# Optimization experiments

Hardware: AMD Instinct MI355X
Metric: run time of the kernel (lower is better)

The kernel has to match this reference:

```python
import jax, jax.numpy as jnp
import numpy as np

B, N, XD = 4, 8192, 256   # batch, seq len, input/kv feature dim
F, H = 512, 8             # features, heads
D = F // H                # per-head dim = 64
EPS = 1e-6                # flax LayerNorm default epsilon


def _layer_norm(t, scale, bias):
    mu = jnp.mean(t, axis=-1, keepdims=True)
    var = jnp.mean(jnp.square(t - mu), axis=-1, keepdims=True)
    return (t - mu) * jax.lax.rsqrt(var + EPS) * scale + bias


def setup_inputs() -> dict:
    key = jax.random.key(0)
    ks = jax.random.split(key, 5)
    return {
        "x": jax.random.normal(ks[0], (B, N, XD), jnp.float32),
        "kv": jax.random.normal(ks[1], (B, N, XD), jnp.float32),
        # linen.initializers.normal(1/x_dim) / normal(1/h_dim)
        "Q": jax.random.normal(ks[2], (XD, F), jnp.float32) * (1.0 / XD),
        "K": jax.random.normal(ks[3], (XD, F), jnp.float32) * (1.0 / XD),
        "V": jax.random.normal(ks[4], (XD, F), jnp.float32) * (1.0 / XD),
        "log_scale": jnp.zeros((F,), jnp.float32),
        "ln_q_scale": jnp.ones((D,), jnp.float32),
        "ln_q_bias": jnp.zeros((D,), jnp.float32),
        "ln_k_scale": jnp.ones((D,), jnp.float32),
        "ln_k_bias": jnp.zeros((D,), jnp.float32),
        "ln_v_scale": jnp.ones((D,), jnp.float32),
        "ln_v_bias": jnp.zeros((D,), jnp.float32),
    }


def reference(x, kv, Q, K, V, log_scale,
              ln_q_scale, ln_q_bias, ln_k_scale, ln_k_bias, ln_v_scale, ln_v_bias):
    # QKV projections (value scaled by exp(log_scale) per feature)
    query = x @ Q                                    # [B, N, F]
    key = kv @ K                                     # [B, N, F]
    value = jnp.exp(log_scale) * (kv @ V)            # [B, N, F]
    # reshape exactly as the source module does
    q = query.reshape(B, H, -1, D)                   # [B, H, N, D]
    k = key.reshape(B, H, -1, D)
    v = value.reshape(B, H, -1, D)
    # per-head LayerNorm over the head dim (layer_norm=True)
    q = _layer_norm(q, ln_q_scale, ln_q_bias)
    k = _layer_norm(k, ln_k_scale, ln_k_bias)
    v = _layer_norm(v, ln_v_scale, ln_v_bias)
    # galerkin linear attention: Q @ (K^T V) / seq_len, no softmax, no NxN scores
    seq_len = k.shape[-2]
    ctx = jnp.einsum('bhnd,bhne->bhde', k, v)        # [B, H, D, D]
    out = jnp.einsum('bhnd,bhde->bhne', q, ctx) / seq_len
    return out.reshape(B, N, F)
```

## Files before the change

kernel.cpp:

```cpp
#include <hip/hip_runtime.h>
#include <stdint.h>

using f32x4  = __attribute__((ext_vector_type(4))) float;
using short8 = __attribute__((ext_vector_type(8))) short;
using u16x4  = __attribute__((ext_vector_type(4))) unsigned short;

#define MFMA(a, b, c) __builtin_amdgcn_mfma_f32_16x16x32_bf16((a), (b), (c), 0, 0, 0)

#define XDIM 256
#define FDIM 512
#define EPS  1e-6f

#define QT_OFF    0u
#define KT_OFF    262144u
#define VT_OFF    524288u
#define CTXT_OFF  786432u
#define PART_OFF  1048576u

static __device__ __forceinline__ unsigned short f2bf(float f) {
  unsigned u = __float_as_uint(f);
  unsigned r = u + 0x7FFFu + ((u >> 16) & 1u);
  return (unsigned short)(r >> 16);
}

static __device__ __forceinline__ void stage_a_full(const float* a_rows, int tid, char* Alds) {
  const int r = tid >> 2, cq = tid & 3;
  const float* src = a_rows + (size_t)r * XDIM + cq * 64;
  char* dst = Alds + r * 528 + cq * 128;
#pragma unroll
  for (int i = 0; i < 4; ++i) {
    float4 f0 = *(const float4*)(src + i * 16);
    float4 f1 = *(const float4*)(src + i * 16 + 4);
    float4 f2 = *(const float4*)(src + i * 16 + 8);
    float4 f3 = *(const float4*)(src + i * 16 + 12);
    short8 v0, v1;
    v0[0] = (short)f2bf(f0.x); v0[1] = (short)f2bf(f0.y);
    v0[2] = (short)f2bf(f0.z); v0[3] = (short)f2bf(f0.w);
    v0[4] = (short)f2bf(f1.x); v0[5] = (short)f2bf(f1.y);
    v0[6] = (short)f2bf(f1.z); v0[7] = (short)f2bf(f1.w);
    v1[0] = (short)f2bf(f2.x); v1[1] = (short)f2bf(f2.y);
    v1[2] = (short)f2bf(f2.z); v1[3] = (short)f2bf(f2.w);
    v1[4] = (short)f2bf(f3.x); v1[5] = (short)f2bf(f3.y);
    v1[6] = (short)f2bf(f3.z); v1[7] = (short)f2bf(f3.w);
    *(short8*)(dst + i * 32)      = v0;
    *(short8*)(dst + i * 32 + 16) = v1;
  }
}

static __device__ __forceinline__ void load_bphase(const char* base, int ks, int lr, int koff,
                                                   short8 b[8]) {
#pragma unroll
  for (int nt = 0; nt < 4; ++nt) {
    const char* r = base + (size_t)(nt * 16 + lr) * 512 + ks * 128 + koff;
    b[nt * 2]     = *(const short8*)(r);
    b[nt * 2 + 1] = *(const short8*)(r + 64);
  }
}

static __device__ __forceinline__ void chunk_layernorm(f32x4 acc[4][4], const float* sc,
                                                       const float* bs, int lane) {
  const int lr = lane & 15;
  float scl[4], bia[4];
#pragma unroll
  for (int nt = 0; nt < 4; ++nt) { scl[nt] = sc[nt * 16 + lr]; bia[nt] = bs[nt * 16 + lr]; }
#pragma unroll
  for (int mt = 0; mt < 4; ++mt) {
#pragma unroll
    for (int j = 0; j < 4; ++j) {
      float a0 = acc[mt][0][j], a1 = acc[mt][1][j], a2 = acc[mt][2][j], a3 = acc[mt][3][j];
      float s  = a0 + a1 + a2 + a3;
      float s2 = a0 * a0 + a1 * a1 + a2 * a2 + a3 * a3;
#pragma unroll
      for (int off = 1; off < 16; off <<= 1) {
        s  += __shfl_xor(s, off, 16);
        s2 += __shfl_xor(s2, off, 16);
      }
      const float mu  = s * (1.0f / 64.0f);
      const float var = s2 * (1.0f / 64.0f) - mu * mu;
      const float rs  = rsqrtf(var + EPS);
#pragma unroll
      for (int nt = 0; nt < 4; ++nt)
        acc[mt][nt][j] = (acc[mt][nt][j] - mu) * rs * scl[nt] + bia[nt];
    }
  }
}

__global__ void prep_weights_kernel(const float* __restrict__ Q, const float* __restrict__ K,
                                    const float* __restrict__ V, const float* __restrict__ ls,
                                    unsigned short* __restrict__ Qt, unsigned short* __restrict__ Kt,
                                    unsigned short* __restrict__ Vt) {
  const int flat = blockIdx.x * 256 + threadIdx.x;
  const int mat = flat >> 17;
  const int rem = flat & 131071;
  const int f = rem & 511;
  const int k = rem >> 9;
  if (mat == 0)      Qt[f * 256 + k] = f2bf(Q[k * 512 + f]);
  else if (mat == 1) Kt[f * 256 + k] = f2bf(K[k * 512 + f]);
  else               Vt[f * 256 + k] = f2bf(V[k * 512 + f] * expf(ls[f]));
}

__launch_bounds__(256, 2)
__global__ void kv_ctx_kernel(const float* __restrict__ kv,
                              const unsigned short* __restrict__ Kt,
                              const unsigned short* __restrict__ Vt,
                              const float* __restrict__ lnk_s, const float* __restrict__ lnk_b,
                              const float* __restrict__ lnv_s, const float* __restrict__ lnv_b,
                              float* __restrict__ partials) {
  __shared__ __align__(16) char smem[33792];

  const int tid = threadIdx.x, lane = tid & 63, w = tid >> 6;
  const int bid = blockIdx.x, rb = bid >> 1, nb = bid & 1;
  const int row0 = rb * 64;
  const int lr = lane & 15, lk = lane >> 4;
  const int koff = lk * 16;

  stage_a_full(kv + (size_t)row0 * XDIM, tid, smem);

  const f32x4 z4 = {0.f, 0.f, 0.f, 0.f};
  f32x4 acck[4][4], accv[4][4];
#pragma unroll
  for (int i = 0; i < 4; ++i)
#pragma unroll
    for (int j = 0; j < 4; ++j) { acck[i][j] = z4; accv[i][j] = z4; }

  const char* kbase = (const char*)Kt + (size_t)(nb * 256 + w * 64) * 512;
  const char* vbase = (const char*)Vt + (size_t)(nb * 256 + w * 64) * 512;

  short8 bufK[8], bufV[8];
  load_bphase(kbase, 0, lr, koff, bufK);
  load_bphase(vbase, 0, lr, koff, bufV);

  __syncthreads();

#pragma unroll
  for (int ks = 0; ks < 4; ++ks) {
    short8 a0[4], a1[4];
#pragma unroll
    for (int mt = 0; mt < 4; ++mt) {
      const char* ar = smem + (mt * 16 + lr) * 528 + ks * 128;
      a0[mt] = *(const short8*)(ar + koff);
      a1[mt] = *(const short8*)(ar + 64 + koff);
    }
#pragma unroll
    for (int mt = 0; mt < 4; ++mt)
#pragma unroll
      for (int nt = 0; nt < 4; ++nt) {
        acck[mt][nt] = MFMA(a0[mt], bufK[nt * 2],     acck[mt][nt]);
        acck[mt][nt] = MFMA(a1[mt], bufK[nt * 2 + 1], acck[mt][nt]);
      }
    if (ks < 3) load_bphase(kbase, ks + 1, lr, koff, bufK);
#pragma unroll
    for (int mt = 0; mt < 4; ++mt)
#pragma unroll
      for (int nt = 0; nt < 4; ++nt) {
        accv[mt][nt] = MFMA(a0[mt], bufV[nt * 2],     accv[mt][nt]);
        accv[mt][nt] = MFMA(a1[mt], bufV[nt * 2 + 1], accv[mt][nt]);
      }
    if (ks < 3) load_bphase(vbase, ks + 1, lr, koff, bufV);
  }

  chunk_layernorm(acck, lnk_s, lnk_b, lane);
  chunk_layernorm(accv, lnv_s, lnv_b, lane);

  char* knT = smem;
  char* vnT = smem + 16384;
  f32x4 cacc[4];
#pragma unroll
  for (int i = 0; i < 4; ++i) cacc[i] = z4;
  const int drow = w * 16 + lr;

#pragma unroll
  for (int half = 0; half < 2; ++half) {
    __syncthreads();
    if ((w >> 1) == half) {
      const int tb2 = (w & 1) * 128;
#pragma unroll
      for (int mt = 0; mt < 4; ++mt) {
        const int tb = tb2 + mt * 32 + lk * 8;
#pragma unroll
        for (int nt = 0; nt < 4; ++nt) {
          const int d = nt * 16 + lr;
          u16x4 pk, pv;
#pragma unroll
          for (int j = 0; j < 4; ++j) {
            pk[j] = f2bf(acck[mt][nt][j]);
            pv[j] = f2bf(accv[mt][nt][j]);
          }
          const int boff = d * 256 + (tb ^ ((d & 7) << 4));
          *(u16x4*)(knT + boff) = pk;
          *(u16x4*)(vnT + boff) = pv;
        }
      }
    }
    __syncthreads();
#pragma unroll
    for (int s = 0; s < 4; ++s) {
      const short8 a = *(const short8*)(knT + drow * 256 + ((s * 64 + koff) ^ ((drow & 7) << 4)));
#pragma unroll
      for (int nt = 0; nt < 4; ++nt) {
        const int e = nt * 16 + lr;
        const short8 b = *(const short8*)(vnT + e * 256 + ((s * 64 + koff) ^ ((e & 7) << 4)));
        cacc[nt] = MFMA(a, b, cacc[nt]);
      }
    }
  }

  float* pout = partials + (size_t)bid * 4096;
#pragma unroll
  for (int nt = 0; nt < 4; ++nt)
#pragma unroll
    for (int j = 0; j < 4; ++j)
      pout[(w * 16 + lk * 4 + j) * 64 + nt * 16 + lr] = cacc[nt][j];
}

__global__ void reduce_ctx_kernel(const float* __restrict__ partials,
                                  unsigned short* __restrict__ ctxTg) {
  const int bid = blockIdx.x, t = threadIdx.x;
  const int gg = bid >> 3, sl = bid & 7;
  const float* base = partials + (size_t)gg * 32 * 4096;
#pragma unroll
  for (int rep = 0; rep < 2; ++rep) {
    const int idx = sl * 512 + rep * 256 + t;
    float acc = 0.f;
#pragma unroll 8
    for (int p = 0; p < 32; ++p) acc += base[(size_t)p * 4096 + idx];
    const int d = idx >> 6, e = idx & 63;
    ctxTg[(size_t)gg * 4096 + e * 64 + d] = f2bf(acc * (1.0f / 8192.0f));
  }
}

__launch_bounds__(256, 3)
__global__ void q_out_kernel(const float* __restrict__ x, const unsigned short* __restrict__ Qt,
                             const unsigned short* __restrict__ ctxTg,
                             const float* __restrict__ lnq_s, const float* __restrict__ lnq_b,
                             float* __restrict__ out) {
  __shared__ __align__(16) char smem[43008];

  const int tid = threadIdx.x, lane = tid & 63, w = tid >> 6;
  const int bid = blockIdx.x, rb = bid >> 1, nb = bid & 1;
  const int row0 = rb * 64;
  const int g = row0 >> 10;
  const int lr = lane & 15, lk = lane >> 4;
  const int koff = lk * 16;
  char* ctxT = smem + 33792;

  stage_a_full(x + (size_t)row0 * XDIM, tid, smem);

  {
    const unsigned short* src = ctxTg + (size_t)g * 4096 + (tid >> 2) * 64 + (tid & 3) * 16;
    char* dst = ctxT + (tid >> 2) * 144 + (tid & 3) * 32;
    *(short8*)dst        = *(const short8*)(src);
    *(short8*)(dst + 16) = *(const short8*)(src + 8);
  }

  const f32x4 z4 = {0.f, 0.f, 0.f, 0.f};
  f32x4 acc[4][4];
#pragma unroll
  for (int i = 0; i < 4; ++i)
#pragma unroll
    for (int j = 0; j < 4; ++j) acc[i][j] = z4;

  const char* qbase = (const char*)Qt + (size_t)(nb * 256 + w * 64) * 512;

  __syncthreads();

#pragma unroll
  for (int ks = 0; ks < 4; ++ks) {
    short8 b0[8];
    load_bphase(qbase, ks, lr, koff, b0);
    short8 a0[4], a1[4];
#pragma unroll
    for (int mt = 0; mt < 4; ++mt) {
      const char* ar = smem + (mt * 16 + lr) * 528 + ks * 128;
      a0[mt] = *(const short8*)(ar + koff);
      a1[mt] = *(const short8*)(ar + 64 + koff);
    }
#pragma unroll
    for (int mt = 0; mt < 4; ++mt)
#pragma unroll
      for (int nt = 0; nt < 4; ++nt)
        acc[mt][nt] = MFMA(a0[mt], b0[nt * 2], acc[mt][nt]);
#pragma unroll
    for (int mt = 0; mt < 4; ++mt)
#pragma unroll
      for (int nt = 0; nt < 4; ++nt)
        acc[mt][nt] = MFMA(a1[mt], b0[nt * 2 + 1], acc[mt][nt]);
  }

  chunk_layernorm(acc, lnq_s, lnq_b, lane);

  __syncthreads();

  char* A2 = smem + w * 8192;
#pragma unroll
  for (int mt = 0; mt < 4; ++mt)
#pragma unroll
    for (int j = 0; j < 4; ++j) {
      const int m = mt * 16 + lk * 4 + j;
      const int sw = (m & 7) << 4;
#pragma unroll
      for (int nt = 0; nt < 4; ++nt) {
        const int d = nt * 16 + lr;
        *(unsigned short*)(A2 + m * 128 + ((d * 2) ^ sw)) = f2bf(acc[mt][nt][j]);
      }
    }
  __syncthreads();

  f32x4 o[4][4];
#pragma unroll
  for (int i = 0; i < 4; ++i)
#pragma unroll
    for (int j = 0; j < 4; ++j) o[i][j] = z4;

#pragma unroll
  for (int s = 0; s < 2; ++s) {
    short8 a[4], b[4];
#pragma unroll
    for (int mt = 0; mt < 4; ++mt) {
      const int m = mt * 16 + lr;
      a[mt] = *(const short8*)(A2 + m * 128 + ((s * 64 + koff) ^ ((m & 7) << 4)));
    }
#pragma unroll
    for (int nt = 0; nt < 4; ++nt)
      b[nt] = *(const short8*)(ctxT + (nt * 16 + lr) * 144 + s * 64 + koff);
#pragma unroll
    for (int mt = 0; mt < 4; ++mt)
#pragma unroll
      for (int nt = 0; nt < 4; ++nt)
        o[mt][nt] = MFMA(a[mt], b[nt], o[mt][nt]);
  }

#pragma unroll
  for (int mt = 0; mt < 4; ++mt)
#pragma unroll
    for (int nt = 0; nt < 4; ++nt)
#pragma unroll
      for (int j = 0; j < 4; ++j) {
        const int n = mt * 16 + lk * 4 + j;
        out[(size_t)(row0 + n) * FDIM + nb * 256 + w * 64 + nt * 16 + lr] = o[mt][nt][j];
      }
}

extern "C" void kernel_launch(void* const* d_in, const int* in_sizes, int n_in,
                              void* d_out, int out_size, void* d_ws, size_t ws_size,
                              hipStream_t stream) {
  (void)in_sizes; (void)n_in; (void)out_size; (void)ws_size;
  const float* x     = (const float*)d_in[0];
  const float* kv    = (const float*)d_in[1];
  const float* Q     = (const float*)d_in[2];
  const float* K     = (const float*)d_in[3];
  const float* V     = (const float*)d_in[4];
  const float* ls    = (const float*)d_in[5];
  const float* lnq_s = (const float*)d_in[6];
  const float* lnq_b = (const float*)d_in[7];
  const float* lnk_s = (const float*)d_in[8];
  const float* lnk_b = (const float*)d_in[9];
  const float* lnv_s = (const float*)d_in[10];
  const float* lnv_b = (const float*)d_in[11];
  float* out = (float*)d_out;

  char* ws = (char*)d_ws;
  unsigned short* Qt   = (unsigned short*)(ws + QT_OFF);
  unsigned short* Kt   = (unsigned short*)(ws + KT_OFF);
  unsigned short* Vt   = (unsigned short*)(ws + VT_OFF);
  unsigned short* ctxT = (unsigned short*)(ws + CTXT_OFF);
  float* partials      = (float*)(ws + PART_OFF);

  prep_weights_kernel<<<1536, 256, 0, stream>>>(Q, K, V, ls, Qt, Kt, Vt);
  kv_ctx_kernel<<<1024, 256, 0, stream>>>(kv, Kt, Vt, lnk_s, lnk_b, lnv_s, lnv_b, partials);
  reduce_ctx_kernel<<<256, 256, 0, stream>>>(partials, ctxT);
  q_out_kernel<<<1024, 256, 0, stream>>>(x, Qt, ctxT, lnq_s, lnq_b, out);
}
```

Before: 111.6 us.

## Pre-convert activations to swizzled bf16 and stage them via async global-to-LDS loads

A prep pass now converts x and kv to bf16 in a swizzled row layout in the workspace. The projection kernels then stage rows straight into LDS with global_load_lds instead of converting fp32 per block. Tiles are split across 2x2 waves over 128-column slices, which doubles the grid and allows higher occupancy. In exchange it adds an extra full read and write of the activations in a separate pass, and doubles the partials that the reduction has to sum.

```diff
diff --git a/kernel.cpp b/kernel.cpp
--- a/kernel.cpp
+++ b/kernel.cpp
@@ -6,6 +6,8 @@
 using u16x4  = __attribute__((ext_vector_type(4))) unsigned short;
 
 #define MFMA(a, b, c) __builtin_amdgcn_mfma_f32_16x16x32_bf16((a), (b), (c), 0, 0, 0)
+#define GLOBAL_AS __attribute__((address_space(1)))
+#define LDS_AS    __attribute__((address_space(3)))
 
 #define XDIM 256
 #define FDIM 512
@@ -15,7 +17,9 @@
 #define KT_OFF    262144u
 #define VT_OFF    524288u
 #define CTXT_OFF  786432u
-#define PART_OFF  1048576u
+#define KVB_OFF   1048576u
+#define XB_OFF    17825792u
+#define PART_OFF  34603008u
 
 static __device__ __forceinline__ unsigned short f2bf(float f) {
   unsigned u = __float_as_uint(f);
@@ -23,48 +27,29 @@
   return (unsigned short)(r >> 16);
 }
 
-static __device__ __forceinline__ void stage_a_full(const float* a_rows, int tid, char* Alds) {
-  const int r = tid >> 2, cq = tid & 3;
-  const float* src = a_rows + (size_t)r * XDIM + cq * 64;
-  char* dst = Alds + r * 528 + cq * 128;
-#pragma unroll
-  for (int i = 0; i < 4; ++i) {
-    float4 f0 = *(const float4*)(src + i * 16);
-    float4 f1 = *(const float4*)(src + i * 16 + 4);
-    float4 f2 = *(const float4*)(src + i * 16 + 8);
-    float4 f3 = *(const float4*)(src + i * 16 + 12);
-    short8 v0, v1;
-    v0[0] = (short)f2bf(f0.x); v0[1] = (short)f2bf(f0.y);
-    v0[2] = (short)f2bf(f0.z); v0[3] = (short)f2bf(f0.w);
-    v0[4] = (short)f2bf(f1.x); v0[5] = (short)f2bf(f1.y);
-    v0[6] = (short)f2bf(f1.z); v0[7] = (short)f2bf(f1.w);
-    v1[0] = (short)f2bf(f2.x); v1[1] = (short)f2bf(f2.y);
-    v1[2] = (short)f2bf(f2.z); v1[3] = (short)f2bf(f2.w);
-    v1[4] = (short)f2bf(f3.x); v1[5] = (short)f2bf(f3.y);
-    v1[6] = (short)f2bf(f3.z); v1[7] = (short)f2bf(f3.w);
-    *(short8*)(dst + i * 32)      = v0;
-    *(short8*)(dst + i * 32 + 16) = v1;
-  }
-}
-
-static __device__ __forceinline__ void load_bphase(const char* base, int ks, int lr, int koff,
-                                                   short8 b[8]) {
-#pragma unroll
-  for (int nt = 0; nt < 4; ++nt) {
-    const char* r = base + (size_t)(nt * 16 + lr) * 512 + ks * 128 + koff;
-    b[nt * 2]     = *(const short8*)(r);
-    b[nt * 2 + 1] = *(const short8*)(r + 64);
-  }
-}
-
-static __device__ __forceinline__ void chunk_layernorm(f32x4 acc[4][4], const float* sc,
+static __device__ __forceinline__ void async_copy16(const void* g, void* l) {
+  __builtin_amdgcn_global_load_lds((GLOBAL_AS const void*)g, (LDS_AS void*)l, 16, 0, 0);
+}
+
+static __device__ __forceinline__ void stage_a_async(const unsigned short* src_rows,
+                                                     int w, int lane, char* Alds) {
+#pragma unroll
+  for (int i = 0; i < 8; ++i) {
+    const int r = w * 16 + i * 2 + (lane >> 5);
+    async_copy16(src_rows + (size_t)r * 256 + (lane & 31) * 8,
+                 Alds + (w * 8 + i) * 1024);
+  }
+}
+
+template <int M_REP>
+static __device__ __forceinline__ void chunk_layernorm(f32x4 acc[M_REP][4], const float* sc,
                                                        const float* bs, int lane) {
   const int lr = lane & 15;
   float scl[4], bia[4];
 #pragma unroll
   for (int nt = 0; nt < 4; ++nt) { scl[nt] = sc[nt * 16 + lr]; bia[nt] = bs[nt * 16 + lr]; }
 #pragma unroll
-  for (int mt = 0; mt < 4; ++mt) {
+  for (int mt = 0; mt < M_REP; ++mt) {
 #pragma unroll
     for (int j = 0; j < 4; ++j) {
       float a0 = acc[mt][0][j], a1 = acc[mt][1][j], a2 = acc[mt][2][j], a3 = acc[mt][3][j];
@@ -85,123 +70,141 @@
   }
 }
 
-__global__ void prep_weights_kernel(const float* __restrict__ Q, const float* __restrict__ K,
-                                    const float* __restrict__ V, const float* __restrict__ ls,
-                                    unsigned short* __restrict__ Qt, unsigned short* __restrict__ Kt,
-                                    unsigned short* __restrict__ Vt) {
-  const int flat = blockIdx.x * 256 + threadIdx.x;
-  const int mat = flat >> 17;
-  const int rem = flat & 131071;
-  const int f = rem & 511;
-  const int k = rem >> 9;
-  if (mat == 0)      Qt[f * 256 + k] = f2bf(Q[k * 512 + f]);
-  else if (mat == 1) Kt[f * 256 + k] = f2bf(K[k * 512 + f]);
-  else               Vt[f * 256 + k] = f2bf(V[k * 512 + f] * expf(ls[f]));
-}
-
-__launch_bounds__(256, 2)
-__global__ void kv_ctx_kernel(const float* __restrict__ kv,
+__global__ void prep_kernel(const float* __restrict__ kv, const float* __restrict__ x,
+                            const float* __restrict__ Q, const float* __restrict__ K,
+                            const float* __restrict__ V, const float* __restrict__ ls,
+                            unsigned short* __restrict__ kvb, unsigned short* __restrict__ xb,
+                            unsigned short* __restrict__ Qt, unsigned short* __restrict__ Kt,
+                            unsigned short* __restrict__ Vt) {
+  const int bid = blockIdx.x, tid = threadIdx.x;
+  if (bid < 4096) {
+    const int sel = bid >> 11;
+    const float* src = sel ? x : kv;
+    unsigned short* dst = sel ? xb : kvb;
+    const size_t e16 = ((size_t)(bid & 2047) * 256 + tid) * 16;
+    const int row = (int)(e16 >> 8);
+    const int col = (int)(e16 & 255);
+    const int c0 = col >> 3;
+    const int s = row & 7;
+    const float* sp = src + e16;
+    short8 v0, v1;
+#pragma unroll
+    for (int j = 0; j < 8; ++j) v0[j] = (short)f2bf(sp[j]);
+#pragma unroll
+    for (int j = 0; j < 8; ++j) v1[j] = (short)f2bf(sp[8 + j]);
+    unsigned short* drow = dst + (size_t)row * 256;
+    *(short8*)(drow + ((c0 ^ s) << 3))       = v0;
+    *(short8*)(drow + (((c0 + 1) ^ s) << 3)) = v1;
+  } else {
+    const int flat = (bid - 4096) * 256 + tid;
+    const int mat = flat >> 17;
+    const int rem = flat & 131071;
+    const int f = rem & 511;
+    const int k = rem >> 9;
+    if (mat == 0)      Qt[f * 256 + k] = f2bf(Q[k * 512 + f]);
+    else if (mat == 1) Kt[f * 256 + k] = f2bf(K[k * 512 + f]);
+    else               Vt[f * 256 + k] = f2bf(V[k * 512 + f] * expf(ls[f]));
+  }
+}
+
+__launch_bounds__(256, 3)
+__global__ void kv_ctx_kernel(const unsigned short* __restrict__ kvb,
                               const unsigned short* __restrict__ Kt,
                               const unsigned short* __restrict__ Vt,
                               const float* __restrict__ lnk_s, const float* __restrict__ lnk_b,
                               const float* __restrict__ lnv_s, const float* __restrict__ lnv_b,
                               float* __restrict__ partials) {
-  __shared__ __align__(16) char smem[33792];
+  __shared__ __align__(16) char smem[32768];
 
   const int tid = threadIdx.x, lane = tid & 63, w = tid >> 6;
-  const int bid = blockIdx.x, rb = bid >> 1, nb = bid & 1;
+  const int wr = w >> 1, wc = w & 1;
+  const int bid = blockIdx.x, rb = bid >> 2, nb = bid & 3;
   const int row0 = rb * 64;
   const int lr = lane & 15, lk = lane >> 4;
-  const int koff = lk * 16;
-
-  stage_a_full(kv + (size_t)row0 * XDIM, tid, smem);
+
+  stage_a_async(kvb + (size_t)row0 * 256, w, lane, smem);
 
   const f32x4 z4 = {0.f, 0.f, 0.f, 0.f};
-  f32x4 acck[4][4], accv[4][4];
-#pragma unroll
-  for (int i = 0; i < 4; ++i)
+  f32x4 acck[2][4], accv[2][4];
+#pragma unroll
+  for (int i = 0; i < 2; ++i)
 #pragma unroll
     for (int j = 0; j < 4; ++j) { acck[i][j] = z4; accv[i][j] = z4; }
 
-  const char* kbase = (const char*)Kt + (size_t)(nb * 256 + w * 64) * 512;
-  const char* vbase = (const char*)Vt + (size_t)(nb * 256 + w * 64) * 512;
-
-  short8 bufK[8], bufV[8];
-  load_bphase(kbase, 0, lr, koff, bufK);
-  load_bphase(vbase, 0, lr, koff, bufV);
+  const unsigned short* kb = Kt + (size_t)(nb * 128 + wc * 64) * 256;
+  const unsigned short* vb = Vt + (size_t)(nb * 128 + wc * 64) * 256;
 
   __syncthreads();
 
 #pragma unroll
   for (int ks = 0; ks < 4; ++ks) {
-    short8 a0[4], a1[4];
-#pragma unroll
-    for (int mt = 0; mt < 4; ++mt) {
-      const char* ar = smem + (mt * 16 + lr) * 528 + ks * 128;
-      a0[mt] = *(const short8*)(ar + koff);
-      a1[mt] = *(const short8*)(ar + 64 + koff);
-    }
-#pragma unroll
-    for (int mt = 0; mt < 4; ++mt)
+    short8 bk[8], bv[8];
+#pragma unroll
+    for (int nt = 0; nt < 4; ++nt) {
+      const unsigned short* kr = kb + (size_t)(nt * 16 + lr) * 256 + ks * 64 + lk * 8;
+      const unsigned short* vr = vb + (size_t)(nt * 16 + lr) * 256 + ks * 64 + lk * 8;
+      bk[nt * 2] = *(const short8*)(kr); bk[nt * 2 + 1] = *(const short8*)(kr + 32);
+      bv[nt * 2] = *(const short8*)(vr); bv[nt * 2 + 1] = *(const short8*)(vr + 32);
+    }
+    short8 a0[2], a1[2];
+#pragma unroll
+    for (int mt = 0; mt < 2; ++mt) {
+      const int row = wr * 32 + mt * 16 + lr;
+      const int sw = (row & 7) << 4;
+      a0[mt] = *(const short8*)(smem + row * 512 + ((ks * 128 + lk * 16) ^ sw));
+      a1[mt] = *(const short8*)(smem + row * 512 + ((ks * 128 + 64 + lk * 16) ^ sw));
+    }
+#pragma unroll
+    for (int mt = 0; mt < 2; ++mt)
 #pragma unroll
       for (int nt = 0; nt < 4; ++nt) {
-        acck[mt][nt] = MFMA(a0[mt], bufK[nt * 2],     acck[mt][nt]);
-        acck[mt][nt] = MFMA(a1[mt], bufK[nt * 2 + 1], acck[mt][nt]);
-      }
-    if (ks < 3) load_bphase(kbase, ks + 1, lr, koff, bufK);
-#pragma unroll
-    for (int mt = 0; mt < 4; ++mt)
+        acck[mt][nt] = MFMA(a0[mt], bk[nt * 2],     acck[mt][nt]);
+        acck[mt][nt] = MFMA(a1[mt], bk[nt * 2 + 1], acck[mt][nt]);
+      }
+#pragma unroll
+    for (int mt = 0; mt < 2; ++mt)
 #pragma unroll
       for (int nt = 0; nt < 4; ++nt) {
-        accv[mt][nt] = MFMA(a0[mt], bufV[nt * 2],     accv[mt][nt]);
-        accv[mt][nt] = MFMA(a1[mt], bufV[nt * 2 + 1], accv[mt][nt]);
-      }
-    if (ks < 3) load_bphase(vbase, ks + 1, lr, koff, bufV);
-  }
-
-  chunk_layernorm(acck, lnk_s, lnk_b, lane);
-  chunk_layernorm(accv, lnv_s, lnv_b, lane);
+        accv[mt][nt] = MFMA(a0[mt], bv[nt * 2],     accv[mt][nt]);
+        accv[mt][nt] = MFMA(a1[mt], bv[nt * 2 + 1], accv[mt][nt]);
+      }
+  }
+
+  chunk_layernorm<2>(acck, lnk_s, lnk_b, lane);
+  chunk_layernorm<2>(accv, lnv_s, lnv_b, lane);
 
   char* knT = smem;
   char* vnT = smem + 16384;
+
+  __syncthreads();
+#pragma unroll
+  for (int mt = 0; mt < 2; ++mt) {
+    const int t = wc * 64 + wr * 32 + mt * 16 + lk * 4;
+#pragma unroll
+    for (int nt = 0; nt < 4; ++nt) {
+      const int d = nt * 16 + lr;
+      u16x4 pk, pv;
+#pragma unroll
+      for (int j = 0; j < 4; ++j) { pk[j] = f2bf(acck[mt][nt][j]); pv[j] = f2bf(accv[mt][nt][j]); }
+      const int boff = d * 256 + ((t * 2) ^ ((d & 7) << 4));
+      *(u16x4*)(knT + boff) = pk;
+      *(u16x4*)(vnT + boff) = pv;
+    }
+  }
+  __syncthreads();
+
   f32x4 cacc[4];
 #pragma unroll
   for (int i = 0; i < 4; ++i) cacc[i] = z4;
   const int drow = w * 16 + lr;
-
-#pragma unroll
-  for (int half = 0; half < 2; ++half) {
-    __syncthreads();
-    if ((w >> 1) == half) {
-      const int tb2 = (w & 1) * 128;
-#pragma unroll
-      for (int mt = 0; mt < 4; ++mt) {
-        const int tb = tb2 + mt * 32 + lk * 8;
-#pragma unroll
-        for (int nt = 0; nt < 4; ++nt) {
-          const int d = nt * 16 + lr;
-          u16x4 pk, pv;
-#pragma unroll
-          for (int j = 0; j < 4; ++j) {
-            pk[j] = f2bf(acck[mt][nt][j]);
-            pv[j] = f2bf(accv[mt][nt][j]);
-          }
-          const int boff = d * 256 + (tb ^ ((d & 7) << 4));
-          *(u16x4*)(knT + boff) = pk;
-          *(u16x4*)(vnT + boff) = pv;
-        }
-      }
-    }
-    __syncthreads();
-#pragma unroll
-    for (int s = 0; s < 4; ++s) {
-      const short8 a = *(const short8*)(knT + drow * 256 + ((s * 64 + koff) ^ ((drow & 7) << 4)));
-#pragma unroll
-      for (int nt = 0; nt < 4; ++nt) {
-        const int e = nt * 16 + lr;
-        const short8 b = *(const short8*)(vnT + e * 256 + ((s * 64 + koff) ^ ((e & 7) << 4)));
-        cacc[nt] = MFMA(a, b, cacc[nt]);
-      }
+#pragma unroll
+  for (int s = 0; s < 4; ++s) {
+    const short8 a = *(const short8*)(knT + drow * 256 + ((s * 64 + lk * 16) ^ ((drow & 7) << 4)));
+#pragma unroll
+    for (int nt = 0; nt < 4; ++nt) {
+      const int e = nt * 16 + lr;
+      const short8 b = *(const short8*)(vnT + e * 256 + ((s * 64 + lk * 16) ^ ((e & 7) << 4)));
+      cacc[nt] = MFMA(a, b, cacc[nt]);
     }
   }
 
@@ -217,127 +220,133 @@
                                   unsigned short* __restrict__ ctxTg) {
   const int bid = blockIdx.x, t = threadIdx.x;
   const int gg = bid >> 3, sl = bid & 7;
-  const float* base = partials + (size_t)gg * 32 * 4096;
+  const float* base = partials + (size_t)gg * 64 * 4096;
 #pragma unroll
   for (int rep = 0; rep < 2; ++rep) {
     const int idx = sl * 512 + rep * 256 + t;
     float acc = 0.f;
 #pragma unroll 8
-    for (int p = 0; p < 32; ++p) acc += base[(size_t)p * 4096 + idx];
+    for (int p = 0; p < 64; ++p) acc += base[(size_t)p * 4096 + idx];
     const int d = idx >> 6, e = idx & 63;
     ctxTg[(size_t)gg * 4096 + e * 64 + d] = f2bf(acc * (1.0f / 8192.0f));
   }
 }
 
-__launch_bounds__(256, 3)
-__global__ void q_out_kernel(const float* __restrict__ x, const unsigned short* __restrict__ Qt,
+__launch_bounds__(256, 4)
+__global__ void q_out_kernel(const unsigned short* __restrict__ xb,
+                             const unsigned short* __restrict__ Qt,
                              const unsigned short* __restrict__ ctxTg,
                              const float* __restrict__ lnq_s, const float* __restrict__ lnq_b,
                              float* __restrict__ out) {
-  __shared__ __align__(16) char smem[43008];
+  __shared__ __align__(16) char smem[32768];
 
   const int tid = threadIdx.x, lane = tid & 63, w = tid >> 6;
-  const int bid = blockIdx.x, rb = bid >> 1, nb = bid & 1;
+  const int wr = w >> 1, wc = w & 1;
+  const int bid = blockIdx.x, rb = bid >> 2, nb = bid & 3;
   const int row0 = rb * 64;
   const int g = row0 >> 10;
   const int lr = lane & 15, lk = lane >> 4;
-  const int koff = lk * 16;
-  char* ctxT = smem + 33792;
-
-  stage_a_full(x + (size_t)row0 * XDIM, tid, smem);
+
+  stage_a_async(xb + (size_t)row0 * 256, w, lane, smem);
+
+  const unsigned short* csrc = ctxTg + (size_t)g * 4096 + (tid >> 2) * 64 + (tid & 3) * 16;
+  const short8 c0 = *(const short8*)(csrc);
+  const short8 c1 = *(const short8*)(csrc + 8);
+
+  const f32x4 z4 = {0.f, 0.f, 0.f, 0.f};
+  f32x4 acc[2][4];
+#pragma unroll
+  for (int i = 0; i < 2; ++i)
+#pragma unroll
+    for (int j = 0; j < 4; ++j) acc[i][j] = z4;
+
+  const unsigned short* qb = Qt + (size_t)(nb * 128 + wc * 64) * 256;
+
+  __syncthreads();
+
+#pragma unroll
+  for (int ks = 0; ks < 4; ++ks) {
+    short8 bq[8];
+#pragma unroll
+    for (int nt = 0; nt < 4; ++nt) {
+      const unsigned short* qr = qb + (size_t)(nt * 16 + lr) * 256 + ks * 64 + lk * 8;
+      bq[nt * 2] = *(const short8*)(qr); bq[nt * 2 + 1] = *(const short8*)(qr + 32);
+    }
+    short8 a0[2], a1[2];
+#pragma unroll
+    for (int mt = 0; mt < 2; ++mt) {
+      const int row = wr * 32 + mt * 16 + lr;
+      const int sw = (row & 7) << 4;
+      a0[mt] = *(const short8*)(smem + row * 512 + ((ks * 128 + lk * 16) ^ sw));
+      a1[mt] = *(const short8*)(smem + row * 512 + ((ks * 128 + 64 + lk * 16) ^ sw));
+    }
+#pragma unroll
+    for (int mt = 0; mt < 2; ++mt)
+#pragma unroll
+      for (int nt = 0; nt < 4; ++nt) {
+        acc[mt][nt] = MFMA(a0[mt], bq[nt * 2],     acc[mt][nt]);
+        acc[mt][nt] = MFMA(a1[mt], bq[nt * 2 + 1], acc[mt][nt]);
+      }
+  }
+
+  chunk_layernorm<2>(acc, lnq_s, lnq_b, lane);
+
+  __syncthreads();
+
+  char* A2   = smem;
+  char* ctxT = smem + 16384;
 
   {
-    const unsigned short* src = ctxTg + (size_t)g * 4096 + (tid >> 2) * 64 + (tid & 3) * 16;
     char* dst = ctxT + (tid >> 2) * 144 + (tid & 3) * 32;
-    *(short8*)dst        = *(const short8*)(src);
-    *(short8*)(dst + 16) = *(const short8*)(src + 8);
-  }
-
-  const f32x4 z4 = {0.f, 0.f, 0.f, 0.f};
-  f32x4 acc[4][4];
-#pragma unroll
-  for (int i = 0; i < 4; ++i)
-#pragma unroll
-    for (int j = 0; j < 4; ++j) acc[i][j] = z4;
-
-  const char* qbase = (const char*)Qt + (size_t)(nb * 256 + w * 64) * 512;
-
-  __syncthreads();
-
-#pragma unroll
-  for (int ks = 0; ks < 4; ++ks) {
-    short8 b0[8];
-    load_bphase(qbase, ks, lr, koff, b0);
-    short8 a0[4], a1[4];
-#pragma unroll
-    for (int mt = 0; mt < 4; ++mt) {
-      const char* ar = smem + (mt * 16 + lr) * 528 + ks * 128;
-      a0[mt] = *(const short8*)(ar + koff);
-      a1[mt] = *(const short8*)(ar + 64 + koff);
-    }
-#pragma unroll
-    for (int mt = 0; mt < 4; ++mt)
-#pragma unroll
-      for (int nt = 0; nt < 4; ++nt)
-        acc[mt][nt] = MFMA(a0[mt], b0[nt * 2], acc[mt][nt]);
-#pragma unroll
-    for (int mt = 0; mt < 4; ++mt)
-#pragma unroll
-      for (int nt = 0; nt < 4; ++nt)
-        acc[mt][nt] = MFMA(a1[mt], b0[nt * 2 + 1], acc[mt][nt]);
-  }
-
-  chunk_layernorm(acc, lnq_s, lnq_b, lane);
-
-  __syncthreads();
-
-  char* A2 = smem + w * 8192;
-#pragma unroll
-  for (int mt = 0; mt < 4; ++mt)
+    *(short8*)dst        = c0;
+    *(short8*)(dst + 16) = c1;
+  }
+#pragma unroll
+  for (int mt = 0; mt < 2; ++mt)
 #pragma unroll
     for (int j = 0; j < 4; ++j) {
-      const int m = mt * 16 + lk * 4 + j;
+      const int m = wr * 32 + mt * 16 + lk * 4 + j;
       const int sw = (m & 7) << 4;
 #pragma unroll
       for (int nt = 0; nt < 4; ++nt) {
         const int d = nt * 16 + lr;
-        *(unsigned short*)(A2 + m * 128 + ((d * 2) ^ sw)) = f2bf(acc[mt][nt][j]);
-      }
-    }
-  __syncthreads();
-
-  f32x4 o[4][4];
-#pragma unroll
-  for (int i = 0; i < 4; ++i)
+        *(unsigned short*)(A2 + wc * 8192 + m * 128 + ((d * 2) ^ sw)) = f2bf(acc[mt][nt][j]);
+      }
+    }
+  __syncthreads();
+
+  f32x4 o[2][4];
+#pragma unroll
+  for (int i = 0; i < 2; ++i)
 #pragma unroll
     for (int j = 0; j < 4; ++j) o[i][j] = z4;
 
 #pragma unroll
   for (int s = 0; s < 2; ++s) {
-    short8 a[4], b[4];
-#pragma unroll
-    for (int mt = 0; mt < 4; ++mt) {
-      const int m = mt * 16 + lr;
-      a[mt] = *(const short8*)(A2 + m * 128 + ((s * 64 + koff) ^ ((m & 7) << 4)));
+    short8 a[2], b[4];
+#pragma unroll
+    for (int mt = 0; mt < 2; ++mt) {
+      const int m = wr * 32 + mt * 16 + lr;
+      a[mt] = *(const short8*)(A2 + wc * 8192 + m * 128 + ((s * 64 + lk * 16) ^ ((m & 7) << 4)));
     }
 #pragma unroll
     for (int nt = 0; nt < 4; ++nt)
-      b[nt] = *(const short8*)(ctxT + (nt * 16 + lr) * 144 + s * 64 + koff);
-#pragma unroll
-    for (int mt = 0; mt < 4; ++mt)
+      b[nt] = *(const short8*)(ctxT + (nt * 16 + lr) * 144 + s * 64 + lk * 16);
+#pragma unroll
+    for (int mt = 0; mt < 2; ++mt)
 #pragma unroll
       for (int nt = 0; nt < 4; ++nt)
         o[mt][nt] = MFMA(a[mt], b[nt], o[mt][nt]);
   }
 
 #pragma unroll
-  for (int mt = 0; mt < 4; ++mt)
+  for (int mt = 0; mt < 2; ++mt)
 #pragma unroll
     for (int nt = 0; nt < 4; ++nt)
 #pragma unroll
       for (int j = 0; j < 4; ++j) {
-        const int n = mt * 16 + lk * 4 + j;
-        out[(size_t)(row0 + n) * FDIM + nb * 256 + w * 64 + nt * 16 + lr] = o[mt][nt][j];
+        const int n = wr * 32 + mt * 16 + lk * 4 + j;
+        out[(size_t)(row0 + n) * FDIM + nb * 128 + wc * 64 + nt * 16 + lr] = o[mt][nt][j];
       }
 }
 
@@ -364,10 +373,12 @@
   unsigned short* Kt   = (unsigned short*)(ws + KT_OFF);
   unsigned short* Vt   = (unsigned short*)(ws + VT_OFF);
   unsigned short* ctxT = (unsigned short*)(ws + CTXT_OFF);
+  unsigned short* kvb  = (unsigned short*)(ws + KVB_OFF);
+  unsigned short* xb   = (unsigned short*)(ws + XB_OFF);
   float* partials      = (float*)(ws + PART_OFF);
 
-  prep_weights_kernel<<<1536, 256, 0, stream>>>(Q, K, V, ls, Qt, Kt, Vt);
-  kv_ctx_kernel<<<1024, 256, 0, stream>>>(kv, Kt, Vt, lnk_s, lnk_b, lnv_s, lnv_b, partials);
+  prep_kernel<<<5632, 256, 0, stream>>>(kv, x, Q, K, V, ls, kvb, xb, Qt, Kt, Vt);
+  kv_ctx_kernel<<<2048, 256, 0, stream>>>(kvb, Kt, Vt, lnk_s, lnk_b, lnv_s, lnv_b, partials);
   reduce_ctx_kernel<<<256, 256, 0, stream>>>(partials, ctxT);
-  q_out_kernel<<<1024, 256, 0, stream>>>(x, Qt, ctxT, lnq_s, lnq_b, out);
-}
+  q_out_kernel<<<2048, 256, 0, stream>>>(xb, Qt, ctxT, lnq_s, lnq_b, out);
+}
```

After: 149.7 us. +34.2%, slower.

## Make KV and Q kernels persistent over row tiles with register-prefetched staging

Applied to the files above, without the earlier changes.

Both main kernels now use 512-thread blocks that each loop over eight 64-row tiles instead of one. The next tile's fp32 input is prefetched into registers while MFMAs run on the current tile held in swizzled LDS. Each wave now covers 64 features, so a block spans 128 features. The weight B-fragments are cycled through registers each loop, and the partial context count per group halves, which shrinks the reduce kernel. The aims are to hide global-load latency, cut launch and block-setup overhead, and reduce partial-sum traffic. The cost is fewer blocks (256), so latency hiding relies on the in-loop prefetch and extra barriers per tile.

```diff
diff --git a/kernel.cpp b/kernel.cpp
--- a/kernel.cpp
+++ b/kernel.cpp
@@ -23,65 +23,51 @@
   return (unsigned short)(r >> 16);
 }
 
-static __device__ __forceinline__ void stage_a_full(const float* a_rows, int tid, char* Alds) {
-  const int r = tid >> 2, cq = tid & 3;
-  const float* src = a_rows + (size_t)r * XDIM + cq * 64;
-  char* dst = Alds + r * 528 + cq * 128;
-#pragma unroll
-  for (int i = 0; i < 4; ++i) {
-    float4 f0 = *(const float4*)(src + i * 16);
-    float4 f1 = *(const float4*)(src + i * 16 + 4);
-    float4 f2 = *(const float4*)(src + i * 16 + 8);
-    float4 f3 = *(const float4*)(src + i * 16 + 12);
-    short8 v0, v1;
-    v0[0] = (short)f2bf(f0.x); v0[1] = (short)f2bf(f0.y);
-    v0[2] = (short)f2bf(f0.z); v0[3] = (short)f2bf(f0.w);
-    v0[4] = (short)f2bf(f1.x); v0[5] = (short)f2bf(f1.y);
-    v0[6] = (short)f2bf(f1.z); v0[7] = (short)f2bf(f1.w);
-    v1[0] = (short)f2bf(f2.x); v1[1] = (short)f2bf(f2.y);
-    v1[2] = (short)f2bf(f2.z); v1[3] = (short)f2bf(f2.w);
-    v1[4] = (short)f2bf(f3.x); v1[5] = (short)f2bf(f3.y);
-    v1[6] = (short)f2bf(f3.z); v1[7] = (short)f2bf(f3.w);
-    *(short8*)(dst + i * 32)      = v0;
-    *(short8*)(dst + i * 32 + 16) = v1;
-  }
-}
-
-static __device__ __forceinline__ void load_bphase(const char* base, int ks, int lr, int koff,
-                                                   short8 b[8]) {
+static __device__ __forceinline__ void stage_issue(const float* tile_base, int tid, float4 fv[8]) {
+  const float* p = tile_base + (size_t)(tid >> 3) * XDIM + (tid & 7) * 32;
+#pragma unroll
+  for (int i = 0; i < 8; ++i) fv[i] = *(const float4*)(p + i * 4);
+}
+static __device__ __forceinline__ void stage_write(char* A, int tid, const float4 fv[8]) {
+  const int row = tid >> 3;
+  const int sw = (row & 7) << 4;
+  char* dst = A + row * 512;
+#pragma unroll
+  for (int q = 0; q < 4; ++q) {
+    short8 v;
+    v[0] = (short)f2bf(fv[2 * q].x);     v[1] = (short)f2bf(fv[2 * q].y);
+    v[2] = (short)f2bf(fv[2 * q].z);     v[3] = (short)f2bf(fv[2 * q].w);
+    v[4] = (short)f2bf(fv[2 * q + 1].x); v[5] = (short)f2bf(fv[2 * q + 1].y);
+    v[6] = (short)f2bf(fv[2 * q + 1].z); v[7] = (short)f2bf(fv[2 * q + 1].w);
+    *(short8*)(dst + ((((tid & 7) * 64) + q * 16) ^ sw)) = v;
+  }
+}
+
+static __device__ __forceinline__ void load_b(const char* base, int ks, int lr, int lk, short8 b[8]) {
 #pragma unroll
   for (int nt = 0; nt < 4; ++nt) {
-    const char* r = base + (size_t)(nt * 16 + lr) * 512 + ks * 128 + koff;
+    const char* r = base + (size_t)(nt * 16 + lr) * 512 + ks * 128 + lk * 16;
     b[nt * 2]     = *(const short8*)(r);
     b[nt * 2 + 1] = *(const short8*)(r + 64);
   }
 }
 
-static __device__ __forceinline__ void chunk_layernorm(f32x4 acc[4][4], const float* sc,
-                                                       const float* bs, int lane) {
-  const int lr = lane & 15;
-  float scl[4], bia[4];
-#pragma unroll
-  for (int nt = 0; nt < 4; ++nt) { scl[nt] = sc[nt * 16 + lr]; bia[nt] = bs[nt * 16 + lr]; }
-#pragma unroll
-  for (int mt = 0; mt < 4; ++mt) {
-#pragma unroll
-    for (int j = 0; j < 4; ++j) {
-      float a0 = acc[mt][0][j], a1 = acc[mt][1][j], a2 = acc[mt][2][j], a3 = acc[mt][3][j];
-      float s  = a0 + a1 + a2 + a3;
-      float s2 = a0 * a0 + a1 * a1 + a2 * a2 + a3 * a3;
-#pragma unroll
-      for (int off = 1; off < 16; off <<= 1) {
-        s  += __shfl_xor(s, off, 16);
-        s2 += __shfl_xor(s2, off, 16);
-      }
-      const float mu  = s * (1.0f / 64.0f);
-      const float var = s2 * (1.0f / 64.0f) - mu * mu;
-      const float rs  = rsqrtf(var + EPS);
-#pragma unroll
-      for (int nt = 0; nt < 4; ++nt)
-        acc[mt][nt][j] = (acc[mt][nt][j] - mu) * rs * scl[nt] + bia[nt];
-    }
+static __device__ __forceinline__ void ln4(f32x4 acc[4], const float scl[4], const float bia[4]) {
+#pragma unroll
+  for (int j = 0; j < 4; ++j) {
+    float a0 = acc[0][j], a1 = acc[1][j], a2 = acc[2][j], a3 = acc[3][j];
+    float s  = a0 + a1 + a2 + a3;
+    float s2 = a0 * a0 + a1 * a1 + a2 * a2 + a3 * a3;
+#pragma unroll
+    for (int off = 1; off < 16; off <<= 1) {
+      s  += __shfl_xor(s, off, 16);
+      s2 += __shfl_xor(s2, off, 16);
+    }
+    const float mu  = s * (1.0f / 64.0f);
+    const float var = s2 * (1.0f / 64.0f) - mu * mu;
+    const float rs  = rsqrtf(var + EPS);
+#pragma unroll
+    for (int nt = 0; nt < 4; ++nt) acc[nt][j] = (acc[nt][j] - mu) * rs * scl[nt] + bia[nt];
   }
 }
 
@@ -99,246 +85,227 @@
   else               Vt[f * 256 + k] = f2bf(V[k * 512 + f] * expf(ls[f]));
 }
 
-__launch_bounds__(256, 2)
+__launch_bounds__(512, 2)
 __global__ void kv_ctx_kernel(const float* __restrict__ kv,
                               const unsigned short* __restrict__ Kt,
                               const unsigned short* __restrict__ Vt,
                               const float* __restrict__ lnk_s, const float* __restrict__ lnk_b,
                               const float* __restrict__ lnv_s, const float* __restrict__ lnv_b,
                               float* __restrict__ partials) {
-  __shared__ __align__(16) char smem[33792];
+  __shared__ __align__(16) char smem[49152];
+  char* Abuf = smem;
+  char* knT  = smem + 32768;
+  char* vnT  = smem + 40960;
 
   const int tid = threadIdx.x, lane = tid & 63, w = tid >> 6;
-  const int bid = blockIdx.x, rb = bid >> 1, nb = bid & 1;
-  const int row0 = rb * 64;
+  const int wc = w & 1, wr = w >> 1;
+  const int bid = blockIdx.x, rb = bid >> 2, nb = bid & 3;
+  const int row0 = rb * 512;
   const int lr = lane & 15, lk = lane >> 4;
-  const int koff = lk * 16;
-
-  stage_a_full(kv + (size_t)row0 * XDIM, tid, smem);
+
+  float sk[4], bk_[4], sv[4], bv_[4];
+#pragma unroll
+  for (int nt = 0; nt < 4; ++nt) {
+    sk[nt] = lnk_s[nt * 16 + lr]; bk_[nt] = lnk_b[nt * 16 + lr];
+    sv[nt] = lnv_s[nt * 16 + lr]; bv_[nt] = lnv_b[nt * 16 + lr];
+  }
+
+  const char* kwb = (const char*)Kt + (size_t)(nb * 128 + wc * 64) * 512;
+  const char* vwb = (const char*)Vt + (size_t)(nb * 128 + wc * 64) * 512;
 
   const f32x4 z4 = {0.f, 0.f, 0.f, 0.f};
-  f32x4 acck[4][4], accv[4][4];
-#pragma unroll
-  for (int i = 0; i < 4; ++i)
-#pragma unroll
-    for (int j = 0; j < 4; ++j) { acck[i][j] = z4; accv[i][j] = z4; }
-
-  const char* kbase = (const char*)Kt + (size_t)(nb * 256 + w * 64) * 512;
-  const char* vbase = (const char*)Vt + (size_t)(nb * 256 + w * 64) * 512;
-
-  short8 bufK[8], bufV[8];
-  load_bphase(kbase, 0, lr, koff, bufK);
-  load_bphase(vbase, 0, lr, koff, bufV);
-
+  f32x4 cacc[4];
+#pragma unroll
+  for (int i = 0; i < 4; ++i) cacc[i] = z4;
+
+  float4 fv[8];
+  stage_issue(kv + (size_t)row0 * XDIM, tid, fv);
+  short8 bK[8], bV[8];
+  load_b(kwb, 0, lr, lk, bK);
+  load_b(vwb, 0, lr, lk, bV);
+  stage_write(Abuf, tid, fv);
   __syncthreads();
 
-#pragma unroll
-  for (int ks = 0; ks < 4; ++ks) {
-    short8 a0[4], a1[4];
-#pragma unroll
-    for (int mt = 0; mt < 4; ++mt) {
-      const char* ar = smem + (mt * 16 + lr) * 528 + ks * 128;
-      a0[mt] = *(const short8*)(ar + koff);
-      a1[mt] = *(const short8*)(ar + 64 + koff);
-    }
-#pragma unroll
-    for (int mt = 0; mt < 4; ++mt)
-#pragma unroll
-      for (int nt = 0; nt < 4; ++nt) {
-        acck[mt][nt] = MFMA(a0[mt], bufK[nt * 2],     acck[mt][nt]);
-        acck[mt][nt] = MFMA(a1[mt], bufK[nt * 2 + 1], acck[mt][nt]);
-      }
-    if (ks < 3) load_bphase(kbase, ks + 1, lr, koff, bufK);
-#pragma unroll
-    for (int mt = 0; mt < 4; ++mt)
-#pragma unroll
-      for (int nt = 0; nt < 4; ++nt) {
-        accv[mt][nt] = MFMA(a0[mt], bufV[nt * 2],     accv[mt][nt]);
-        accv[mt][nt] = MFMA(a1[mt], bufV[nt * 2 + 1], accv[mt][nt]);
-      }
-    if (ks < 3) load_bphase(vbase, ks + 1, lr, koff, bufV);
-  }
-
-  chunk_layernorm(acck, lnk_s, lnk_b, lane);
-  chunk_layernorm(accv, lnv_s, lnv_b, lane);
-
-  char* knT = smem;
-  char* vnT = smem + 16384;
-  f32x4 cacc[4];
-#pragma unroll
-  for (int i = 0; i < 4; ++i) cacc[i] = z4;
-  const int drow = w * 16 + lr;
-
-#pragma unroll
-  for (int half = 0; half < 2; ++half) {
-    __syncthreads();
-    if ((w >> 1) == half) {
-      const int tb2 = (w & 1) * 128;
-#pragma unroll
-      for (int mt = 0; mt < 4; ++mt) {
-        const int tb = tb2 + mt * 32 + lk * 8;
+  const int arow = wr * 16 + lr;
+  const int asw = (arow & 7) << 4;
+  const int drow = (w & 3) * 16 + lr;
+  const int dsw = (drow & 7) << 4;
+  const int tq = w >> 2;
+
+  for (int t = 0; t < 8; ++t) {
+    if (t < 7) stage_issue(kv + (size_t)(row0 + (t + 1) * 64) * XDIM, tid, fv);
+
+    f32x4 ak[4], av[4];
+#pragma unroll
+    for (int i = 0; i < 4; ++i) { ak[i] = z4; av[i] = z4; }
+#pragma unroll
+    for (int ks = 0; ks < 4; ++ks) {
+      const char* ap = Abuf + arow * 512;
+      const short8 a0 = *(const short8*)(ap + ((ks * 128 + lk * 16) ^ asw));
+      const short8 a1 = *(const short8*)(ap + ((ks * 128 + 64 + lk * 16) ^ asw));
+#pragma unroll
+      for (int nt = 0; nt < 4; ++nt) {
+        ak[nt] = MFMA(a0, bK[nt * 2],     ak[nt]);
+        ak[nt] = MFMA(a1, bK[nt * 2 + 1], ak[nt]);
+      }
+      load_b(kwb, (ks + 1) & 3, lr, lk, bK);
+#pragma unroll
+      for (int nt = 0; nt < 4; ++nt) {
+        av[nt] = MFMA(a0, bV[nt * 2],     av[nt]);
+        av[nt] = MFMA(a1, bV[nt * 2 + 1], av[nt]);
+      }
+      load_b(vwb, (ks + 1) & 3, lr, lk, bV);
+    }
+
+    ln4(ak, sk, bk_);
+    ln4(av, sv, bv_);
+
+#pragma unroll
+    for (int p = 0; p < 2; ++p) {
+      __syncthreads();
+      if (p == 0 && t < 7) stage_write(Abuf, tid, fv);
+      if (wc == p) {
 #pragma unroll
         for (int nt = 0; nt < 4; ++nt) {
           const int d = nt * 16 + lr;
+          const int boff = d * 128 + ((wr * 32 + lk * 8) ^ ((d & 7) << 4));
           u16x4 pk, pv;
 #pragma unroll
-          for (int j = 0; j < 4; ++j) {
-            pk[j] = f2bf(acck[mt][nt][j]);
-            pv[j] = f2bf(accv[mt][nt][j]);
-          }
-          const int boff = d * 256 + (tb ^ ((d & 7) << 4));
+          for (int j = 0; j < 4; ++j) { pk[j] = f2bf(ak[nt][j]); pv[j] = f2bf(av[nt][j]); }
           *(u16x4*)(knT + boff) = pk;
           *(u16x4*)(vnT + boff) = pv;
         }
       }
-    }
-    __syncthreads();
-#pragma unroll
-    for (int s = 0; s < 4; ++s) {
-      const short8 a = *(const short8*)(knT + drow * 256 + ((s * 64 + koff) ^ ((drow & 7) << 4)));
+      __syncthreads();
+      const short8 a = *(const short8*)(knT + drow * 128 + ((tq * 64 + lk * 16) ^ dsw));
 #pragma unroll
       for (int nt = 0; nt < 4; ++nt) {
         const int e = nt * 16 + lr;
-        const short8 b = *(const short8*)(vnT + e * 256 + ((s * 64 + koff) ^ ((e & 7) << 4)));
+        const short8 b = *(const short8*)(vnT + e * 128 + ((tq * 64 + lk * 16) ^ (((e & 7) << 4))));
         cacc[nt] = MFMA(a, b, cacc[nt]);
       }
     }
   }
 
-  float* pout = partials + (size_t)bid * 4096;
+  float* pout = partials + ((size_t)bid * 2 + tq) * 4096;
 #pragma unroll
   for (int nt = 0; nt < 4; ++nt)
 #pragma unroll
     for (int j = 0; j < 4; ++j)
-      pout[(w * 16 + lk * 4 + j) * 64 + nt * 16 + lr] = cacc[nt][j];
+      pout[((w & 3) * 16 + lk * 4 + j) * 64 + nt * 16 + lr] = cacc[nt][j];
 }
 
 __global__ void reduce_ctx_kernel(const float* __restrict__ partials,
                                   unsigned short* __restrict__ ctxTg) {
   const int bid = blockIdx.x, t = threadIdx.x;
   const int gg = bid >> 3, sl = bid & 7;
-  const float* base = partials + (size_t)gg * 32 * 4096;
+  const float* base = partials + (size_t)gg * 16 * 4096;
 #pragma unroll
   for (int rep = 0; rep < 2; ++rep) {
     const int idx = sl * 512 + rep * 256 + t;
     float acc = 0.f;
-#pragma unroll 8
-    for (int p = 0; p < 32; ++p) acc += base[(size_t)p * 4096 + idx];
+#pragma unroll
+    for (int p = 0; p < 16; ++p) acc += base[(size_t)p * 4096 + idx];
     const int d = idx >> 6, e = idx & 63;
     ctxTg[(size_t)gg * 4096 + e * 64 + d] = f2bf(acc * (1.0f / 8192.0f));
   }
 }
 
-__launch_bounds__(256, 3)
+__launch_bounds__(512, 2)
 __global__ void q_out_kernel(const float* __restrict__ x, const unsigned short* __restrict__ Qt,
                              const unsigned short* __restrict__ ctxTg,
                              const float* __restrict__ lnq_s, const float* __restrict__ lnq_b,
                              float* __restrict__ out) {
-  __shared__ __align__(16) char smem[43008];
+  __shared__ __align__(16) char smem[60416];
+  char* Abuf = smem;
+  char* ctxT = smem + 32768;
+  char* A2   = smem + 41984;
 
   const int tid = threadIdx.x, lane = tid & 63, w = tid >> 6;
-  const int bid = blockIdx.x, rb = bid >> 1, nb = bid & 1;
-  const int row0 = rb * 64;
-  const int g = row0 >> 10;
+  const int wc = w & 1, wr = w >> 1;
+  const int bid = blockIdx.x, rb = bid >> 2, nb = bid & 3;
+  const int row0 = rb * 512;
+  const int g = rb >> 1;
   const int lr = lane & 15, lk = lane >> 4;
-  const int koff = lk * 16;
-  char* ctxT = smem + 33792;
-
-  stage_a_full(x + (size_t)row0 * XDIM, tid, smem);
+
+  float sq[4], bq_[4];
+#pragma unroll
+  for (int nt = 0; nt < 4; ++nt) { sq[nt] = lnq_s[nt * 16 + lr]; bq_[nt] = lnq_b[nt * 16 + lr]; }
+
+  const char* qwb = (const char*)Qt + (size_t)(nb * 128 + wc * 64) * 512;
 
   {
-    const unsigned short* src = ctxTg + (size_t)g * 4096 + (tid >> 2) * 64 + (tid & 3) * 16;
-    char* dst = ctxT + (tid >> 2) * 144 + (tid & 3) * 32;
-    *(short8*)dst        = *(const short8*)(src);
-    *(short8*)(dst + 16) = *(const short8*)(src + 8);
-  }
-
+    const unsigned short* src = ctxTg + (size_t)g * 4096 + (tid >> 3) * 64 + (tid & 7) * 8;
+    *(short8*)(ctxT + (tid >> 3) * 144 + (tid & 7) * 16) = *(const short8*)src;
+  }
+  float4 fv[8];
+  stage_issue(x + (size_t)row0 * XDIM, tid, fv);
+  short8 bQ[8];
+  load_b(qwb, 0, lr, lk, bQ);
+  stage_write(Abuf, tid, fv);
+  __syncthreads();
+
+  const int arow = wr * 16 + lr;
+  const int asw = (arow & 7) << 4;
   const f32x4 z4 = {0.f, 0.f, 0.f, 0.f};
-  f32x4 acc[4][4];
-#pragma unroll
-  for (int i = 0; i < 4; ++i)
-#pragma unroll
-    for (int j = 0; j < 4; ++j) acc[i][j] = z4;
-
-  const char* qbase = (const char*)Qt + (size_t)(nb * 256 + w * 64) * 512;
-
-  __syncthreads();
-
-#pragma unroll
-  for (int ks = 0; ks < 4; ++ks) {
-    short8 b0[8];
-    load_bphase(qbase, ks, lr, koff, b0);
-    short8 a0[4], a1[4];
-#pragma unroll
-    for (int mt = 0; mt < 4; ++mt) {
-      const char* ar = smem + (mt * 16 + lr) * 528 + ks * 128;
-      a0[mt] = *(const short8*)(ar + koff);
-      a1[mt] = *(const short8*)(ar + 64 + koff);
-    }
-#pragma unroll
-    for (int mt = 0; mt < 4; ++mt)
-#pragma unroll
-      for (int nt = 0; nt < 4; ++nt)
-        acc[mt][nt] = MFMA(a0[mt], b0[nt * 2], acc[mt][nt]);
-#pragma unroll
-    for (int mt = 0; mt < 4; ++mt)
-#pragma unroll
-      for (int nt = 0; nt < 4; ++nt)
-        acc[mt][nt] = MFMA(a1[mt], b0[nt * 2 + 1], acc[mt][nt]);
-  }
-
-  chunk_layernorm(acc, lnq_s, lnq_b, lane);
-
-  __syncthreads();
-
-  char* A2 = smem + w * 8192;
-#pragma unroll
-  for (int mt = 0; mt < 4; ++mt)
-#pragma unroll
-    for (int j = 0; j < 4; ++j) {
-      const int m = mt * 16 + lk * 4 + j;
-      const int sw = (m & 7) << 4;
-#pragma unroll
-      for (int nt = 0; nt < 4; ++nt) {
-        const int d = nt * 16 + lr;
-        *(unsigned short*)(A2 + m * 128 + ((d * 2) ^ sw)) = f2bf(acc[mt][nt][j]);
-      }
-    }
-  __syncthreads();
-
-  f32x4 o[4][4];
-#pragma unroll
-  for (int i = 0; i < 4; ++i)
-#pragma unroll
-    for (int j = 0; j < 4; ++j) o[i][j] = z4;
-
-#pragma unroll
-  for (int s = 0; s < 2; ++s) {
-    short8 a[4], b[4];
-#pragma unroll
-    for (int mt = 0; mt < 4; ++mt) {
-      const int m = mt * 16 + lr;
-      a[mt] = *(const short8*)(A2 + m * 128 + ((s * 64 + koff) ^ ((m & 7) << 4)));
-    }
+
+  for (int t = 0; t < 8; ++t) {
+    if (t < 7) stage_issue(x + (size_t)(row0 + (t + 1) * 64) * XDIM, tid, fv);
+
+    f32x4 acc[4];
+#pragma unroll
+    for (int i = 0; i < 4; ++i) acc[i] = z4;
+#pragma unroll
+    for (int ks = 0; ks < 4; ++ks) {
+      const char* ap = Abuf + arow * 512;
+      const short8 a0 = *(const short8*)(ap + ((ks * 128 + lk * 16) ^ asw));
+      const short8 a1 = *(const short8*)(ap + ((ks * 128 + 64 + lk * 16) ^ asw));
+#pragma unroll
+      for (int nt = 0; nt < 4; ++nt) {
+        acc[nt] = MFMA(a0, bQ[nt * 2],     acc[nt]);
+        acc[nt] = MFMA(a1, bQ[nt * 2 + 1], acc[nt]);
+      }
+      load_b(qwb, (ks + 1) & 3, lr, lk, bQ);
+    }
+
+    ln4(acc, sq, bq_);
+
+    __syncthreads();
+    if (t < 7) stage_write(Abuf, tid, fv);
+
+    char* a2 = A2 + wc * 9216;
+#pragma unroll
+    for (int nt = 0; nt < 4; ++nt) {
+      const int d = nt * 16 + lr;
+#pragma unroll
+      for (int j = 0; j < 4; ++j) {
+        const int m = wr * 16 + lk * 4 + j;
+        *(unsigned short*)(a2 + m * 144 + d * 2) = f2bf(acc[nt][j]);
+      }
+    }
+
+    f32x4 o[4];
+#pragma unroll
+    for (int i = 0; i < 4; ++i) o[i] = z4;
+#pragma unroll
+    for (int s = 0; s < 2; ++s) {
+      const short8 a = *(const short8*)(a2 + (wr * 16 + lr) * 144 + s * 64 + lk * 16);
+#pragma unroll
+      for (int nt = 0; nt < 4; ++nt) {
+        const short8 b = *(const short8*)(ctxT + (nt * 16 + lr) * 144 + s * 64 + lk * 16);
+        o[nt] = MFMA(a, b, o[nt]);
+      }
+    }
+
+    const int rbase = row0 + t * 64 + wr * 16;
 #pragma unroll
     for (int nt = 0; nt < 4; ++nt)
-      b[nt] = *(const short8*)(ctxT + (nt * 16 + lr) * 144 + s * 64 + koff);
-#pragma unroll
-    for (int mt = 0; mt < 4; ++mt)
-#pragma unroll
-      for (int nt = 0; nt < 4; ++nt)
-        o[mt][nt] = MFMA(a[mt], b[nt], o[mt][nt]);
-  }
-
-#pragma unroll
-  for (int mt = 0; mt < 4; ++mt)
-#pragma unroll
-    for (int nt = 0; nt < 4; ++nt)
-#pragma unroll
-      for (int j = 0; j < 4; ++j) {
-        const int n = mt * 16 + lk * 4 + j;
-        out[(size_t)(row0 + n) * FDIM + nb * 256 + w * 64 + nt * 16 + lr] = o[mt][nt][j];
-      }
+#pragma unroll
+      for (int j = 0; j < 4; ++j)
+        out[(size_t)(rbase + lk * 4 + j) * FDIM + nb * 128 + wc * 64 + nt * 16 + lr] = o[nt][j];
+
+    __syncthreads();
+  }
 }
 
 extern "C" void kernel_launch(void* const* d_in, const int* in_sizes, int n_in,
@@ -367,7 +334,7 @@
   float* partials      = (float*)(ws + PART_OFF);
 
   prep_weights_kernel<<<1536, 256, 0, stream>>>(Q, K, V, ls, Qt, Kt, Vt);
-  kv_ctx_kernel<<<1024, 256, 0, stream>>>(kv, Kt, Vt, lnk_s, lnk_b, lnv_s, lnv_b, partials);
+  kv_ctx_kernel<<<256, 512, 0, stream>>>(kv, Kt, Vt, lnk_s, lnk_b, lnv_s, lnv_b, partials);
   reduce_ctx_kernel<<<256, 256, 0, stream>>>(partials, ctxT);
-  q_out_kernel<<<1024, 256, 0, stream>>>(x, Qt, ctxT, lnq_s, lnq_b, out);
-}
+  q_out_kernel<<<256, 512, 0, stream>>>(x, Qt, ctxT, lnq_s, lnq_b, out);
+}
```

Measured after the change: 243.9 us. 2.19x slower.
